# Kernel optimization log

Measured on AMD Instinct MI355X. Metric: run time of the kernel, lower is better.

Reference implementation:

```python
import jax, jax.numpy as jnp
import numpy as np


def sparsemax(x, axis=-1):
    axis = axis % x.ndim
    d = x.shape[axis]
    # sort descending along axis
    x_sorted = -jnp.sort(-x, axis=axis)
    x_cum = jnp.cumsum(x_sorted, axis=axis)
    k = jnp.arange(1, d + 1, dtype=x.dtype)
    k_shape = [1] * axis + [d] + [1] * (x.ndim - axis - 1)
    k_exp = k.reshape(k_shape)
    # support size: number of entries satisfying 1 + k*z_sorted > cumsum
    constraint = 1 + k_exp * x_sorted > x_cum
    k_x = jnp.sum(constraint, axis=axis, dtype=jnp.int32)
    k_x = jnp.maximum(k_x, 1)
    idx = jnp.expand_dims(k_x - 1, axis=axis)
    tau_sum = jnp.take_along_axis(x_cum, idx, axis=axis)
    tau = (tau_sum - 1) / idx.astype(x.dtype).__add__(1)  # (tau_sum - 1) / k_x
    out = jax.nn.relu(x - tau.astype(x.dtype))
    out = jnp.where(jnp.isfinite(out), out, jnp.asarray(jnp.nan, dtype=x.dtype))
    return out


def setup_inputs() -> dict:
    key = jax.random.key(0)
    x = jax.random.normal(key, (4096, 8192), dtype=jnp.float32)
    return {"x": x}


def reference(x) -> jnp.ndarray:
    return sparsemax(x, axis=-1)
```

## Files before the change

kernel.cpp:

```cpp
#include <hip/hip_runtime.h>


constexpr int D       = 8192;
constexpr int THREADS = 256;
constexpr int F4PT    = D / (THREADS * 4);

__device__ __forceinline__ void block_reduce2(float& a, float& b, float* lds) {
    #pragma unroll
    for (int off = 1; off < 64; off <<= 1) {
        a += __shfl_xor(a, off, 64);
        b += __shfl_xor(b, off, 64);
    }
    const int wave = threadIdx.x >> 6;
    const int lane = threadIdx.x & 63;
    __syncthreads();
    if (lane == 0) { lds[wave] = a; lds[4 + wave] = b; }
    __syncthreads();
    a = (lds[0] + lds[1]) + (lds[2] + lds[3]);
    b = (lds[4] + lds[5]) + (lds[6] + lds[7]);
}

__global__ __launch_bounds__(THREADS, 4)
void sparsemax_kernel(const float* __restrict__ x, float* __restrict__ out) {
    __shared__ float lds[8];
    const long long row = blockIdx.x;
    const float* __restrict__ xr  = x   + row * (long long)D;
    float* __restrict__       orw = out + row * (long long)D;
    const int tid = threadIdx.x;

    float4 v[F4PT];
    #pragma unroll
    for (int i = 0; i < F4PT; ++i)
        v[i] = reinterpret_cast<const float4*>(xr)[tid + i * THREADS];

    float s = 0.f, z = 0.f;
    #pragma unroll
    for (int i = 0; i < F4PT; ++i)
        s += (v[i].x + v[i].y) + (v[i].z + v[i].w);
    block_reduce2(s, z, lds);

    float tau   = (s - 1.f) / (float)D;
    float kprev = (float)D;

    for (int it = 0; it < 64; ++it) {
        float S = 0.f, K = 0.f;
        #pragma unroll
        for (int i = 0; i < F4PT; ++i) {
            float e;
            e = v[i].x; if (e > tau) { S += e; K += 1.f; }
            e = v[i].y; if (e > tau) { S += e; K += 1.f; }
            e = v[i].z; if (e > tau) { S += e; K += 1.f; }
            e = v[i].w; if (e > tau) { S += e; K += 1.f; }
        }
        block_reduce2(S, K, lds);
        if (K < 0.5f) break;
        tau = (S - 1.f) / K;
        if (K == kprev) break;
        kprev = K;
    }

    #pragma unroll
    for (int i = 0; i < F4PT; ++i) {
        float4 o;
        o.x = fmaxf(v[i].x - tau, 0.f);
        o.y = fmaxf(v[i].y - tau, 0.f);
        o.z = fmaxf(v[i].z - tau, 0.f);
        o.w = fmaxf(v[i].w - tau, 0.f);
        reinterpret_cast<float4*>(orw)[tid + i * THREADS] = o;
    }
}

extern "C" void kernel_launch(void* const* d_in, const int* in_sizes, int n_in,
                              void* d_out, int out_size, void* d_ws, size_t ws_size,
                              hipStream_t stream) {
    const float* x = (const float*)d_in[0];
    float* out = (float*)d_out;
    const int rows = in_sizes[0] / D;
    sparsemax_kernel<<<rows, THREADS, 0, stream>>>(x, out);
}
```

Baseline: 237.5 us.

## Prune sparsemax candidates above max-1 into LDS before fixed-point iteration

The kernel computes the row max, using the fact that tau >= max-1. It then gathers the elements above max-1 into a small shared-memory candidate list through an atomic counter and runs the Michelot-style fixed-point iteration on at most four candidates per thread instead of 32 elements per thread. The row is now staged in LDS rather than held in registers, and output stores are nontemporal. This adds a 32KB LDS footprint per block, which can limit occupancy, plus LDS atomics, and keeps a full-row fallback for when the candidate count overflows.

```diff
diff --git a/kernel.cpp b/kernel.cpp
--- a/kernel.cpp
+++ b/kernel.cpp
@@ -1,11 +1,16 @@
 #include <hip/hip_runtime.h>
+#include <float.h>
 
 
 constexpr int D       = 8192;
 constexpr int THREADS = 256;
 constexpr int F4PT    = D / (THREADS * 4);
+constexpr int VPT     = D / THREADS;
+constexpr int CAP     = 1024;
 
-__device__ __forceinline__ void block_reduce2(float& a, float& b, float* lds) {
+typedef float f32x4 __attribute__((ext_vector_type(4)));
+
+__device__ __forceinline__ void block_reduce2(float& a, float& b, float* red) {
     #pragma unroll
     for (int off = 1; off < 64; off <<= 1) {
         a += __shfl_xor(a, off, 64);
@@ -14,59 +19,105 @@
     const int wave = threadIdx.x >> 6;
     const int lane = threadIdx.x & 63;
     __syncthreads();
-    if (lane == 0) { lds[wave] = a; lds[4 + wave] = b; }
+    if (lane == 0) { red[wave] = a; red[4 + wave] = b; }
     __syncthreads();
-    a = (lds[0] + lds[1]) + (lds[2] + lds[3]);
-    b = (lds[4] + lds[5]) + (lds[6] + lds[7]);
+    a = (red[0] + red[1]) + (red[2] + red[3]);
+    b = (red[4] + red[5]) + (red[6] + red[7]);
 }
 
 __global__ __launch_bounds__(THREADS, 4)
 void sparsemax_kernel(const float* __restrict__ x, float* __restrict__ out) {
-    __shared__ float lds[8];
-    const long long row = blockIdx.x;
-    const float* __restrict__ xr  = x   + row * (long long)D;
-    float* __restrict__       orw = out + row * (long long)D;
-    const int tid = threadIdx.x;
+    __shared__ float row[D];
+    __shared__ float cands[CAP];
+    __shared__ float red[8];
+    __shared__ int   cnt;
 
-    float4 v[F4PT];
+    const long long r = blockIdx.x;
+    const f32x4* __restrict__ xr4 = reinterpret_cast<const f32x4*>(x + r * (long long)D);
+    f32x4* __restrict__       or4 = reinterpret_cast<f32x4*>(out + r * (long long)D);
+    f32x4* row4 = reinterpret_cast<f32x4*>(row);
+    const int tid  = threadIdx.x;
+    const int wave = tid >> 6, lane = tid & 63;
+
+    if (tid == 0) cnt = 0;
+
+    float m = -FLT_MAX;
     #pragma unroll
-    for (int i = 0; i < F4PT; ++i)
-        v[i] = reinterpret_cast<const float4*>(xr)[tid + i * THREADS];
+    for (int i = 0; i < F4PT; ++i) {
+        f32x4 t = xr4[tid + i * THREADS];
+        row4[tid + i * THREADS] = t;
+        m = fmaxf(m, fmaxf(fmaxf(t.x, t.y), fmaxf(t.z, t.w)));
+    }
+    #pragma unroll
+    for (int off = 1; off < 64; off <<= 1)
+        m = fmaxf(m, __shfl_xor(m, off, 64));
+    __syncthreads();
+    if (lane == 0) red[wave] = m;
+    __syncthreads();
+    m = fmaxf(fmaxf(red[0], red[1]), fmaxf(red[2], red[3]));
+    const float thr = m - 1.0f;
 
-    float s = 0.f, z = 0.f;
     #pragma unroll
-    for (int i = 0; i < F4PT; ++i)
-        s += (v[i].x + v[i].y) + (v[i].z + v[i].w);
-    block_reduce2(s, z, lds);
+    for (int j = 0; j < VPT; ++j) {
+        float v = row[tid + j * THREADS];
+        if (v > thr) {
+            int p = atomicAdd(&cnt, 1);
+            if (p < CAP) cands[p] = v;
+        }
+    }
+    __syncthreads();
+    const int n = cnt;
 
-    float tau   = (s - 1.f) / (float)D;
-    float kprev = (float)D;
-
-    for (int it = 0; it < 64; ++it) {
-        float S = 0.f, K = 0.f;
+    float tau;
+    if (n <= CAP) {
+        float c0 = (tid               < n) ? cands[tid              ] : -FLT_MAX;
+        float c1 = (tid +     THREADS < n) ? cands[tid +     THREADS] : -FLT_MAX;
+        float c2 = (tid + 2 * THREADS < n) ? cands[tid + 2 * THREADS] : -FLT_MAX;
+        float c3 = (tid + 3 * THREADS < n) ? cands[tid + 3 * THREADS] : -FLT_MAX;
+        tau = thr;
+        float kprev = -1.0f;
+        for (int it = 0; it < 32; ++it) {
+            float S = 0.f, K = 0.f;
+            if (c0 > tau) { S += c0; K += 1.f; }
+            if (c1 > tau) { S += c1; K += 1.f; }
+            if (c2 > tau) { S += c2; K += 1.f; }
+            if (c3 > tau) { S += c3; K += 1.f; }
+            block_reduce2(S, K, red);
+            tau = (S - 1.f) / K;
+            if (K == kprev) break;
+            kprev = K;
+        }
+    } else {
+        float s = 0.f, z = 0.f;
         #pragma unroll
-        for (int i = 0; i < F4PT; ++i) {
-            float e;
-            e = v[i].x; if (e > tau) { S += e; K += 1.f; }
-            e = v[i].y; if (e > tau) { S += e; K += 1.f; }
-            e = v[i].z; if (e > tau) { S += e; K += 1.f; }
-            e = v[i].w; if (e > tau) { S += e; K += 1.f; }
+        for (int j = 0; j < VPT; ++j) s += row[tid + j * THREADS];
+        block_reduce2(s, z, red);
+        tau = (s - 1.f) / (float)D;
+        float kprev = (float)D;
+        for (int it = 0; it < 64; ++it) {
+            float S = 0.f, K = 0.f;
+            #pragma unroll
+            for (int j = 0; j < VPT; ++j) {
+                float v = row[tid + j * THREADS];
+                if (v > tau) { S += v; K += 1.f; }
+            }
+            block_reduce2(S, K, red);
+            if (K < 0.5f) break;
+            tau = (S - 1.f) / K;
+            if (K == kprev) break;
+            kprev = K;
         }
-        block_reduce2(S, K, lds);
-        if (K < 0.5f) break;
-        tau = (S - 1.f) / K;
-        if (K == kprev) break;
-        kprev = K;
     }
 
     #pragma unroll
     for (int i = 0; i < F4PT; ++i) {
-        float4 o;
-        o.x = fmaxf(v[i].x - tau, 0.f);
-        o.y = fmaxf(v[i].y - tau, 0.f);
-        o.z = fmaxf(v[i].z - tau, 0.f);
-        o.w = fmaxf(v[i].w - tau, 0.f);
-        reinterpret_cast<float4*>(orw)[tid + i * THREADS] = o;
+        f32x4 t = row4[tid + i * THREADS];
+        f32x4 o;
+        o.x = fmaxf(t.x - tau, 0.f);
+        o.y = fmaxf(t.y - tau, 0.f);
+        o.z = fmaxf(t.z - tau, 0.f);
+        o.w = fmaxf(t.w - tau, 0.f);
+        __builtin_nontemporal_store(o, &or4[tid + i * THREADS]);
     }
 }
 
```

New measurement: 235.4 us. About the same (-0.9%).
